# Optimization experiments

Hardware: AMD Instinct MI355X
Metric: run time of the kernel (lower is better)

## Reference

```python
import jax, jax.numpy as jnp
import numpy as np

SOS_TOKEN_ID = 1
SUMMARY_LEN = 16  # decoder produces SUMMARY_LEN - 1 steps


def setup_inputs() -> dict:
    key = jax.random.key(0)
    ks = jax.random.split(key, 10)
    B, L, D, Vc, Vs = 256, 200, 512, 50000, 20000
    s = 0.05  # keep activations in a sane range for tanh/softmax
    return {
        "method_code": jax.random.randint(ks[0], (B, L), 0, Vc),
        "code_emb_table": jax.random.normal(ks[1], (Vc, D), jnp.float32) * s,
        "summary_emb_table": jax.random.normal(ks[2], (Vs, D), jnp.float32) * s,
        "w_ih": jax.random.normal(ks[3], (4 * D, D), jnp.float32) * s,
        "w_hh": jax.random.normal(ks[4], (4 * D, D), jnp.float32) * s,
        "b_ih": jnp.zeros((4 * D,), jnp.float32),
        "b_hh": jnp.zeros((4 * D,), jnp.float32),
        "t_w": jax.random.normal(ks[5], (D, D), jnp.float32) * s,
        "t_b": jnp.zeros((D,), jnp.float32),
        "h_w": jax.random.normal(ks[6], (D, D), jnp.float32) * s,
        "h_b": jnp.zeros((D,), jnp.float32),
        "p_w": jax.random.normal(ks[7], (Vs, D), jnp.float32) * s,
        "p_b": jnp.zeros((Vs,), jnp.float32),
    }


def reference(method_code, code_emb_table, summary_emb_table,
              w_ih, w_hh, b_ih, b_hh, t_w, t_b, h_w, h_b, p_w, p_b):
    B = method_code.shape[0]
    D = code_emb_table.shape[1]
    code_emb = code_emb_table[method_code]  # [B, L, D]

    def step(carry, _):
        h, c, prev_tok = carry
        x = summary_emb_table[prev_tok]                       # [B, D]
        # torch LSTMCell: gates ordered i, f, g, o
        gates = x @ w_ih.T + b_ih + h @ w_hh.T + b_hh          # [B, 4D]
        i_g, f_g, g_g, o_g = jnp.split(gates, 4, axis=-1)
        c_new = jax.nn.sigmoid(f_g) * c + jax.nn.sigmoid(i_g) * jnp.tanh(g_g)
        h_new = jax.nn.sigmoid(o_g) * jnp.tanh(c_new)
        # dot-product attention over code embeddings
        attn = jax.nn.softmax(jnp.einsum('bd,bld->bl', h_new, code_emb), axis=-1)
        t = jnp.einsum('bl,bld->bd', attn, code_emb)           # [B, D]
        pre = t @ t_w.T + t_b + h_new @ h_w.T + h_b            # [B, D]
        logits = jnp.tanh(pre) @ p_w.T + p_b                   # [B, V]
        next_tok = jnp.argmax(logits, axis=-1)                 # greedy feedback
        return (h_new, c_new, next_tok), logits

    h0 = jnp.zeros((B, D), code_emb.dtype)
    c0 = jnp.zeros((B, D), code_emb.dtype)
    prev0 = jnp.full((B,), SOS_TOKEN_ID, dtype=method_code.dtype)
    _, logits_seq = jax.lax.scan(step, (h0, c0, prev0), None, length=SUMMARY_LEN - 1)
    return jnp.transpose(logits_seq, (1, 0, 2))  # [B, summary_len-1, V]
```

## Files before the change

### kernel.cpp

```cpp
#include <hip/hip_runtime.h>
#include <math.h>

#define BB 256
#define LL 200
#define DD 512
#define VS 20000
#define VS_PAD 20224
#define STEPS 15

typedef __attribute__((ext_vector_type(8))) short bf16x8;
typedef __attribute__((ext_vector_type(4))) float f32x4;

__device__ __forceinline__ unsigned int mono_key(float f) {
    unsigned int u = __float_as_uint(f);
    return (u & 0x80000000u) ? ~u : (u | 0x80000000u);
}

__device__ __forceinline__ unsigned short f2bf_rn(float x) {
    unsigned int u = __float_as_uint(x);
    unsigned int r = (u + 0x7FFFu + ((u >> 16) & 1u)) >> 16;
    return (unsigned short)r;
}
__device__ __forceinline__ float bf2f(unsigned short b) {
    return __uint_as_float((unsigned int)b << 16);
}

__device__ __forceinline__ void split_store8(float4 v0, float4 v1,
    unsigned short* __restrict__ hi, unsigned short* __restrict__ lo)
{
    ushort4 h0, h1, l0, l1;
    h0.x = f2bf_rn(v0.x); l0.x = f2bf_rn(v0.x - bf2f(h0.x));
    h0.y = f2bf_rn(v0.y); l0.y = f2bf_rn(v0.y - bf2f(h0.y));
    h0.z = f2bf_rn(v0.z); l0.z = f2bf_rn(v0.z - bf2f(h0.z));
    h0.w = f2bf_rn(v0.w); l0.w = f2bf_rn(v0.w - bf2f(h0.w));
    h1.x = f2bf_rn(v1.x); l1.x = f2bf_rn(v1.x - bf2f(h1.x));
    h1.y = f2bf_rn(v1.y); l1.y = f2bf_rn(v1.y - bf2f(h1.y));
    h1.z = f2bf_rn(v1.z); l1.z = f2bf_rn(v1.z - bf2f(h1.z));
    h1.w = f2bf_rn(v1.w); l1.w = f2bf_rn(v1.w - bf2f(h1.w));
    *(ushort4*)hi = h0; *(ushort4*)(hi + 4) = h1;
    *(ushort4*)lo = l0; *(ushort4*)(lo + 4) = l1;
}

__device__ __forceinline__ void split_frag(float4 v0, float4 v1, bf16x8& hi, bf16x8& lo)
{
    float vv[8] = {v0.x, v0.y, v0.z, v0.w, v1.x, v1.y, v1.z, v1.w};
    #pragma unroll
    for (int j = 0; j < 8; j++) {
        unsigned short hb = f2bf_rn(vv[j]);
        hi[j] = (short)hb;
        lo[j] = (short)f2bf_rn(vv[j] - bf2f(hb));
    }
}

__global__ __launch_bounds__(256) void init_keys_kernel(unsigned long long* keys) {
    keys[threadIdx.x] = (unsigned long long)(unsigned int)(~1u);
}


__global__ __launch_bounds__(256) void split_pw_kernel(
    const float* __restrict__ p_w, unsigned short* __restrict__ p_hi,
    unsigned short* __restrict__ p_lo)
{
    size_t q = (size_t)blockIdx.x * 256 + threadIdx.x;
    int P   = (int)(q >> 10);
    int rem = (int)(q & 1023);
    int c   = rem >> 6;
    int l   = rem & 63;
    int row = P * 16 + (l & 15);
    int ks  = c * 32 + (l >> 4) * 8;
    float4 v0 = {0.f, 0.f, 0.f, 0.f}, v1 = {0.f, 0.f, 0.f, 0.f};
    if (row < VS) {
        const float* src = p_w + (size_t)row * DD + ks;
        v0 = *(const float4*)src;
        v1 = *(const float4*)(src + 4);
    }
    split_store8(v0, v1, p_hi + q * 8, p_lo + q * 8);
}

template <int PERM>
__global__ __launch_bounds__(256) void split_wcat_kernel(
    const float* __restrict__ s0, const float* __restrict__ s1,
    unsigned short* __restrict__ wh, unsigned short* __restrict__ wl)
{
    size_t q = (size_t)blockIdx.x * 256 + threadIdx.x;
    int P   = (int)(q >> 11);
    int rem = (int)(q & 2047);
    int c   = rem >> 6;
    int l   = rem & 63;
    int row;
    if (PERM) row = (P & 3) * 512 + (P >> 2) * 16 + (l & 15);
    else      row = P * 16 + (l & 15);
    int k   = c * 32 + (l >> 4) * 8;
    const float* src = (k < 512) ? (s0 + (size_t)row * DD + k)
                                 : (s1 + (size_t)row * DD + (k - 512));
    float4 v0 = *(const float4*)src;
    float4 v1 = *(const float4*)(src + 4);
    split_store8(v0, v1, wh + q * 8, wl + q * 8);
}

__global__ __launch_bounds__(256) void gates_lstm_kernel(
    const float* __restrict__ sum_emb, const unsigned long long* __restrict__ keys,
    const unsigned short* __restrict__ hin_hi, const unsigned short* __restrict__ hin_lo,
    const unsigned short* __restrict__ w1h, const unsigned short* __restrict__ w1l,
    const float* __restrict__ bi, const float* __restrict__ bh,
    float* __restrict__ c, float* __restrict__ h,
    unsigned short* __restrict__ hout_hi, unsigned short* __restrict__ hout_lo)
{
    const int tid  = threadIdx.x;
    const int lane = tid & 63;
    const int wav  = tid >> 6;
    const int col = lane & 15;
    const int kg  = lane >> 4;
    const int m0  = (blockIdx.y * 4 + wav) * 16;
    const int nt  = blockIdx.x;

    unsigned int tok = ~(unsigned int)(keys[m0 + col] & 0xFFFFFFFFull);

    const size_t ahoff = (size_t)(m0 >> 4) * 8192 + (size_t)lane * 8;
    const size_t boff  = (size_t)(nt * 4) * 16384 + (size_t)lane * 8;

    f32x4 acc[4];
    #pragma unroll
    for (int g = 0; g < 4; g++) acc[g] = (f32x4){0.f, 0.f, 0.f, 0.f};

    bf16x8 fa_h[2], fa_l[2], fb_h[2][4], fb_l[2][4];

#define GL_LOAD(C, BUF)                                                            \
    {                                                                              \
        if ((C) < 16) {                                                            \
            const float* s_ = sum_emb + (size_t)tok * DD + (C) * 32 + kg * 8;      \
            float4 v0 = *(const float4*)s_;                                        \
            float4 v1 = *(const float4*)(s_ + 4);                                  \
            split_frag(v0, v1, fa_h[BUF], fa_l[BUF]);                              \
        } else {                                                                   \
            fa_h[BUF] = *(const bf16x8*)(hin_hi + ahoff + ((C) - 16) * 512);       \
            fa_l[BUF] = *(const bf16x8*)(hin_lo + ahoff + ((C) - 16) * 512);       \
        }                                                                          \
        _Pragma("unroll")                                                          \
        for (int g = 0; g < 4; g++) {                                              \
            fb_h[BUF][g] = *(const bf16x8*)(w1h + boff + (size_t)g * 16384 + (C) * 512); \
            fb_l[BUF][g] = *(const bf16x8*)(w1l + boff + (size_t)g * 16384 + (C) * 512); \
        }                                                                          \
    }

    GL_LOAD(0, 0);
    #pragma unroll
    for (int cc = 0; cc < 32; cc++) {
        const int cur = cc & 1, nxt = cur ^ 1;
        if (cc < 31) GL_LOAD(cc + 1, nxt);
        #pragma unroll
        for (int g = 0; g < 4; g++) {
            acc[g] = __builtin_amdgcn_mfma_f32_16x16x32_bf16(fa_h[cur], fb_h[cur][g], acc[g], 0, 0, 0);
            acc[g] = __builtin_amdgcn_mfma_f32_16x16x32_bf16(fa_h[cur], fb_l[cur][g], acc[g], 0, 0, 0);
            acc[g] = __builtin_amdgcn_mfma_f32_16x16x32_bf16(fa_l[cur], fb_h[cur][g], acc[g], 0, 0, 0);
        }
    }
#undef GL_LOAD

    const int feat = nt * 16 + col;
    float bias[4];
    #pragma unroll
    for (int g = 0; g < 4; g++)
        bias[g] = bi[g * 512 + feat] + bh[g * 512 + feat];

    #pragma unroll
    for (int r = 0; r < 4; r++) {
        const int b = m0 + kg * 4 + r;
        float vi = acc[0][r] + bias[0];
        float vf = acc[1][r] + bias[1];
        float vg = acc[2][r] + bias[2];
        float vo = acc[3][r] + bias[3];
        double ig = 1.0 / (1.0 + exp(-(double)vi));
        double fg = 1.0 / (1.0 + exp(-(double)vf));
        double gv = tanh((double)vg);
        double og = 1.0 / (1.0 + exp(-(double)vo));
        size_t cidx = (size_t)b * DD + feat;
        double cn = fg * (double)c[cidx] + ig * gv;
        double hn = og * tanh(cn);
        c[cidx] = (float)cn;
        float hf = (float)hn;
        h[cidx] = hf;
        size_t hidx = (size_t)(b >> 4) * 8192 + (size_t)(feat >> 5) * 512
                    + (size_t)(((feat >> 3) & 3) * 16 + (b & 15)) * 8 + (feat & 7);
        unsigned short hb2 = f2bf_rn(hf);
        hout_hi[hidx] = hb2;
        hout_lo[hidx] = f2bf_rn(hf - bf2f(hb2));
    }
}

__global__ __launch_bounds__(256) void pre_kernel(
    const unsigned short* __restrict__ t_hi, const unsigned short* __restrict__ t_lo,
    const unsigned short* __restrict__ h_hi, const unsigned short* __restrict__ h_lo,
    const unsigned short* __restrict__ w2h, const unsigned short* __restrict__ w2l,
    const float* __restrict__ tb, const float* __restrict__ hbv,
    unsigned short* __restrict__ o_hi, unsigned short* __restrict__ o_lo)
{
    const int tid  = threadIdx.x;
    const int lane = tid & 63;
    const int wav  = tid >> 6;
    const int col  = lane & 15;
    const int kg   = lane >> 4;
    const int m0   = blockIdx.y * 16;
    const int n0   = blockIdx.x * 32;

    const unsigned short* ah = (wav < 2) ? t_hi : h_hi;
    const unsigned short* al = (wav < 2) ? t_lo : h_lo;
    const size_t aoff = (size_t)(m0 >> 4) * 8192 + (size_t)lane * 8
                      + (size_t)((wav & 1) * 8) * 512;
    const size_t boff = (size_t)(n0 >> 4) * 16384 + (size_t)lane * 8
                      + (size_t)(wav * 8) * 512;

    f32x4 acc[2];
    acc[0] = (f32x4){0.f, 0.f, 0.f, 0.f};
    acc[1] = (f32x4){0.f, 0.f, 0.f, 0.f};

    bf16x8 fa_h[2], fa_l[2], fb_h[2][2], fb_l[2][2];
    fa_h[0] = *(const bf16x8*)(ah + aoff);
    fa_l[0] = *(const bf16x8*)(al + aoff);
    #pragma unroll
    for (int g = 0; g < 2; g++) {
        fb_h[0][g] = *(const bf16x8*)(w2h + boff + (size_t)g * 16384);
        fb_l[0][g] = *(const bf16x8*)(w2l + boff + (size_t)g * 16384);
    }
    #pragma unroll
    for (int cc = 0; cc < 8; cc++) {
        const int cur = cc & 1, nxt = cur ^ 1;
        if (cc < 7) {
            const int off = (cc + 1) * 512;
            fa_h[nxt] = *(const bf16x8*)(ah + aoff + off);
            fa_l[nxt] = *(const bf16x8*)(al + aoff + off);
            #pragma unroll
            for (int g = 0; g < 2; g++) {
                fb_h[nxt][g] = *(const bf16x8*)(w2h + boff + (size_t)g * 16384 + off);
                fb_l[nxt][g] = *(const bf16x8*)(w2l + boff + (size_t)g * 16384 + off);
            }
        }
        #pragma unroll
        for (int g = 0; g < 2; g++) {
            acc[g] = __builtin_amdgcn_mfma_f32_16x16x32_bf16(fa_h[cur], fb_h[cur][g], acc[g], 0, 0, 0);
            acc[g] = __builtin_amdgcn_mfma_f32_16x16x32_bf16(fa_h[cur], fb_l[cur][g], acc[g], 0, 0, 0);
            acc[g] = __builtin_amdgcn_mfma_f32_16x16x32_bf16(fa_l[cur], fb_h[cur][g], acc[g], 0, 0, 0);
        }
    }

    __shared__ float psum[4][16][32];
    #pragma unroll
    for (int g = 0; g < 2; g++)
        #pragma unroll
        for (int r = 0; r < 4; r++)
            psum[wav][kg * 4 + r][g * 16 + col] = acc[g][r];
    __syncthreads();

    #pragma unroll
    for (int e = 0; e < 2; e++) {
        const int idx  = tid * 2 + e;
        const int row  = idx >> 5, coln = idx & 31;
        const int b    = m0 + row;
        const int n    = n0 + coln;
        float accs = (psum[0][row][coln] + psum[1][row][coln])
                   + (psum[2][row][coln] + psum[3][row][coln]);
        float val = accs + (tb[n] + hbv[n]);
        float v2 = (float)tanh((double)val);
        int P = b >> 4, colb = b & 15;
        int cc2 = n >> 5, kgg = (n >> 3) & 3, jj = n & 7;
        size_t oidx = (size_t)P * 8192 + (size_t)cc2 * 512
                    + (size_t)(kgg * 16 + colb) * 8 + jj;
        unsigned short hb = f2bf_rn(v2);
        o_hi[oidx] = hb;
        o_lo[oidx] = f2bf_rn(v2 - bf2f(hb));
    }
}

template <int NCH, int EPI, int WPB>
__global__ __launch_bounds__(64 * WPB, 3) void mfma_gemm(
    const unsigned short* __restrict__ a0h, const unsigned short* __restrict__ a0l,
    const unsigned short* __restrict__ a1h, const unsigned short* __restrict__ a1l,
    const unsigned short* __restrict__ bmh, const unsigned short* __restrict__ bml,
    const float* __restrict__ bias0, const float* __restrict__ bias1,
    float* __restrict__ outp,
    unsigned short* __restrict__ o_hi, unsigned short* __restrict__ o_lo,
    unsigned long long* __restrict__ keys, int s)
{
    const int tid  = threadIdx.x;
    const int lane = tid & 63;
    const int wav  = tid >> 6;
    const int col = lane & 15;
    const int kg  = lane >> 4;
    const int m0 = (blockIdx.y * WPB + wav) * 32;
    const int n0 = blockIdx.x * 64;

    const size_t aoff = (size_t)(m0 >> 4) * 8192 + (size_t)lane * 8;
    const size_t boff = (size_t)(n0 >> 4) * (NCH * 512) + (size_t)lane * 8;

    f32x4 acc[2][4];
    #pragma unroll
    for (int f = 0; f < 2; f++)
        #pragma unroll
        for (int g = 0; g < 4; g++)
            acc[f][g] = (f32x4){0.f, 0.f, 0.f, 0.f};

    bf16x8 fah[2][2], fal[2][2], fbh[2][4], fbl[2][4];

#define LOAD_CHUNK(C, BUF)                                                         \
    {                                                                              \
        const unsigned short* ah_ = ((NCH == 16) || ((C) < 16)) ? a0h : a1h;       \
        const unsigned short* al_ = ((NCH == 16) || ((C) < 16)) ? a0l : a1l;       \
        const int cc_ = (C) & 15;                                                  \
        _Pragma("unroll")                                                          \
        for (int f = 0; f < 2; f++) {                                              \
            fah[BUF][f] = *(const bf16x8*)(ah_ + aoff + (size_t)f * 8192 + cc_ * 512); \
            fal[BUF][f] = *(const bf16x8*)(al_ + aoff + (size_t)f * 8192 + cc_ * 512); \
        }                                                                          \
        _Pragma("unroll")                                                          \
        for (int g = 0; g < 4; g++) {                                              \
            fbh[BUF][g] = *(const bf16x8*)(bmh + boff + (size_t)g * (NCH * 512) + (C) * 512); \
            fbl[BUF][g] = *(const bf16x8*)(bml + boff + (size_t)g * (NCH * 512) + (C) * 512); \
        }                                                                          \
    }

    LOAD_CHUNK(0, 0);
    #pragma unroll
    for (int c = 0; c < NCH; c++) {
        const int cur = c & 1, nxt = cur ^ 1;
        if (c < NCH - 1) LOAD_CHUNK(c + 1, nxt);
        #pragma unroll
        for (int f = 0; f < 2; f++)
            #pragma unroll
            for (int g = 0; g < 4; g++) {
                acc[f][g] = __builtin_amdgcn_mfma_f32_16x16x32_bf16(fah[cur][f], fbh[cur][g], acc[f][g], 0, 0, 0);
                acc[f][g] = __builtin_amdgcn_mfma_f32_16x16x32_bf16(fah[cur][f], fbl[cur][g], acc[f][g], 0, 0, 0);
                acc[f][g] = __builtin_amdgcn_mfma_f32_16x16x32_bf16(fal[cur][f], fbh[cur][g], acc[f][g], 0, 0, 0);
            }
    }
#undef LOAD_CHUNK

    float bias[4];
    #pragma unroll
    for (int g = 0; g < 4; g++) {
        int v = n0 + g * 16 + col;
        bias[g] = (v < VS) ? bias0[v] : 0.f;
    }

    #pragma unroll
    for (int f = 0; f < 2; f++) {
        #pragma unroll
        for (int r = 0; r < 4; r++) {
            const int b = m0 + f * 16 + kg * 4 + r;
            float* orow = outp + ((size_t)b * STEPS + s) * VS;
            unsigned long long kmax = 0ull;
            #pragma unroll
            for (int g = 0; g < 4; g++) {
                int v = n0 + g * 16 + col;
                float val = acc[f][g][r] + bias[g];
                if (v < VS) {
                    orow[v] = val;
                    unsigned long long key =
                        ((unsigned long long)mono_key(val) << 32) |
                        (unsigned long long)(unsigned int)(~v);
                    if (key > kmax) kmax = key;
                }
            }
            #pragma unroll
            for (int mk = 1; mk < 16; mk <<= 1) {
                unsigned long long o = __shfl_xor(kmax, mk, 64);
                if (o > kmax) kmax = o;
            }
            if (col == 0) {
                if (kmax > *(volatile unsigned long long*)&keys[b])
                    atomicMax(&keys[b], kmax);
            }
        }
    }
}

__global__ __launch_bounds__(512) void attn_kernel(
    const int* __restrict__ method_code, const float* __restrict__ code_emb,
    const float* __restrict__ h, unsigned short* __restrict__ t_hi,
    unsigned short* __restrict__ t_lo, unsigned long long* __restrict__ keys)
{
    const int b = blockIdx.x;
    const int tid = threadIdx.x;
    const int lane = tid & 63, wave = tid >> 6;

    __shared__ float sc[LL];
    __shared__ int   rows[LL];
    __shared__ float fred[256];
    __shared__ double dred[256];
    __shared__ float ts[DD];
    __shared__ float part[8][DD];

    if (tid < LL) rows[tid] = method_code[b * LL + tid];
    if (tid == 0) keys[b] = 0ull;
    const float* hb = h + (size_t)b * DD;
    float4 h0 = *(const float4*)(hb + lane * 8);
    float4 h1 = *(const float4*)(hb + lane * 8 + 4);
    __syncthreads();

    for (int l = wave; l < LL; l += 8) {
        const float* e = code_emb + (size_t)rows[l] * DD + lane * 8;
        float4 e0 = *(const float4*)e;
        float4 e1 = *(const float4*)(e + 4);
        float p = h0.x * e0.x + h0.y * e0.y + h0.z * e0.z + h0.w * e0.w
                + h1.x * e1.x + h1.y * e1.y + h1.z * e1.z + h1.w * e1.w;
        #pragma unroll
        for (int m = 1; m < 64; m <<= 1) p += __shfl_xor(p, m, 64);
        if (lane == 0) sc[l] = p;
    }
    __syncthreads();

    if (tid < 256) fred[tid] = (tid < LL) ? sc[tid] : -INFINITY;
    __syncthreads();
    for (int s2 = 128; s2 > 0; s2 >>= 1) {
        if (tid < s2) fred[tid] = fmaxf(fred[tid], fred[tid + s2]);
        __syncthreads();
    }
    float smax = fred[0];
    __syncthreads();
    double w = (tid < LL) ? exp((double)sc[tid] - (double)smax) : 0.0;
    if (tid < 256) dred[tid] = w;
    __syncthreads();
    for (int s2 = 128; s2 > 0; s2 >>= 1) {
        if (tid < s2) dred[tid] += dred[tid + s2];
        __syncthreads();
    }
    double ssum = dred[0];
    __syncthreads();
    if (tid < LL) sc[tid] = (float)(w / ssum);
    __syncthreads();

    float pa[8] = {0.f, 0.f, 0.f, 0.f, 0.f, 0.f, 0.f, 0.f};
    for (int l = wave; l < LL; l += 8) {
        float wl = sc[l];
        const float* e = code_emb + (size_t)rows[l] * DD + lane * 8;
        float4 e0 = *(const float4*)e;
        float4 e1 = *(const float4*)(e + 4);
        pa[0] = fmaf(wl, e0.x, pa[0]); pa[1] = fmaf(wl, e0.y, pa[1]);
        pa[2] = fmaf(wl, e0.z, pa[2]); pa[3] = fmaf(wl, e0.w, pa[3]);
        pa[4] = fmaf(wl, e1.x, pa[4]); pa[5] = fmaf(wl, e1.y, pa[5]);
        pa[6] = fmaf(wl, e1.z, pa[6]); pa[7] = fmaf(wl, e1.w, pa[7]);
    }
    #pragma unroll
    for (int j = 0; j < 8; j++) part[wave][lane * 8 + j] = pa[j];
    __syncthreads();

    {
        const int d = tid;
        float v01 = part[0][d] + part[1][d];
        float v23 = part[2][d] + part[3][d];
        float v45 = part[4][d] + part[5][d];
        float v67 = part[6][d] + part[7][d];
        ts[d] = (v01 + v23) + (v45 + v67);
    }
    __syncthreads();

    if (tid < 64) {
        const int cc = tid >> 2, kgg = tid & 3;
        const float* src = ts + cc * 32 + kgg * 8;
        float4 v0 = *(const float4*)src;
        float4 v1 = *(const float4*)(src + 4);
        size_t base = (size_t)(b >> 4) * 8192 + (size_t)cc * 512
                    + (size_t)(kgg * 16 + (b & 15)) * 8;
        split_store8(v0, v1, t_hi + base, t_lo + base);
    }
}

extern "C" void kernel_launch(void* const* d_in, const int* in_sizes, int n_in,
                              void* d_out, int out_size, void* d_ws, size_t ws_size,
                              hipStream_t stream)
{
    const int*   method_code = (const int*)d_in[0];
    const float* code_emb    = (const float*)d_in[1];
    const float* sum_emb     = (const float*)d_in[2];
    const float* w_ih        = (const float*)d_in[3];
    const float* w_hh        = (const float*)d_in[4];
    const float* b_ih        = (const float*)d_in[5];
    const float* b_hh        = (const float*)d_in[6];
    const float* t_w         = (const float*)d_in[7];
    const float* t_b         = (const float*)d_in[8];
    const float* h_w         = (const float*)d_in[9];
    const float* h_b         = (const float*)d_in[10];
    const float* p_w         = (const float*)d_in[11];
    const float* p_b         = (const float*)d_in[12];
    float* out = (float*)d_out;

    float* h     = (float*)d_ws;
    float* c     = h + BB * DD;
    unsigned long long* keys = (unsigned long long*)(c + BB * DD);
    unsigned short* a_hi   = (unsigned short*)(keys + BB);
    unsigned short* a_lo   = a_hi   + BB * DD;
    unsigned short* t_hi   = a_lo   + BB * DD;
    unsigned short* t_lo   = t_hi   + BB * DD;
    unsigned short* hp0_hi = t_lo   + BB * DD;
    unsigned short* hp0_lo = hp0_hi + BB * DD;
    unsigned short* hp1_hi = hp0_lo + BB * DD;
    unsigned short* hp1_lo = hp1_hi + BB * DD;
    unsigned short* w1_hi  = hp1_lo + BB * DD;
    unsigned short* w1_lo  = w1_hi  + (size_t)2048 * 1024;
    unsigned short* w2_hi  = w1_lo  + (size_t)2048 * 1024;
    unsigned short* w2_lo  = w2_hi  + (size_t)512 * 1024;
    unsigned short* p_hi   = w2_lo  + (size_t)512 * 1024;
    unsigned short* p_lo   = p_hi   + (size_t)VS_PAD * DD;

    hipMemsetAsync(h, 0, (size_t)2 * BB * DD * sizeof(float), stream);
    hipMemsetAsync(hp0_hi, 0, (size_t)2 * BB * DD * sizeof(unsigned short), stream);
    init_keys_kernel<<<1, 256, 0, stream>>>(keys);
    split_pw_kernel<<<(VS_PAD * 64) / 256, 256, 0, stream>>>(p_w, p_hi, p_lo);
    split_wcat_kernel<1><<<1024, 256, 0, stream>>>(w_ih, w_hh, w1_hi, w1_lo);
    split_wcat_kernel<0><<<256, 256, 0, stream>>>(t_w, h_w, w2_hi, w2_lo);

    for (int s = 0; s < STEPS; s++) {
        const unsigned short* hin_hi  = (s & 1) ? hp1_hi : hp0_hi;
        const unsigned short* hin_lo  = (s & 1) ? hp1_lo : hp0_lo;
        unsigned short*       hout_hi = (s & 1) ? hp0_hi : hp1_hi;
        unsigned short*       hout_lo = (s & 1) ? hp0_lo : hp1_lo;

        gates_lstm_kernel<<<dim3(32, 4), 256, 0, stream>>>(
            sum_emb, keys, hin_hi, hin_lo, w1_hi, w1_lo, b_ih, b_hh,
            c, h, hout_hi, hout_lo);
        attn_kernel<<<256, 512, 0, stream>>>(method_code, code_emb, h, t_hi, t_lo, keys);
        pre_kernel<<<dim3(16, 16), 256, 0, stream>>>(
            t_hi, t_lo, hout_hi, hout_lo, w2_hi, w2_lo, t_b, h_b, a_hi, a_lo);
        mfma_gemm<16, 2, 4><<<dim3(316, 2), 256, 0, stream>>>(
            a_hi, a_lo, nullptr, nullptr, p_hi, p_lo, p_b, nullptr,
            out, nullptr, nullptr, keys, s);
    }
}
```

Measured before the change: 2.068 ms.

## Fuse attention score and weighted-sum passes with online softmax

Replaces the two-pass attention (scores, block softmax reductions, then a second gather of code embeddings) with a single pass that keeps a running max and sum per wave and rescales the partial weighted sums. Per-wave partials are merged once at the end with exp rescaling. This removes the second read of 200 gathered embedding rows and the many barrier-heavy tree reductions. In exchange it adds per-iteration double-precision exp and conditional rescaling, and the float rounding order changes slightly.

```diff
diff --git a/kernel.cpp b/kernel.cpp
--- a/kernel.cpp
+++ b/kernel.cpp
@@ -382,12 +382,11 @@
     const int tid = threadIdx.x;
     const int lane = tid & 63, wave = tid >> 6;
 
-    __shared__ float sc[LL];
-    __shared__ int   rows[LL];
-    __shared__ float fred[256];
-    __shared__ double dred[256];
-    __shared__ float ts[DD];
-    __shared__ float part[8][DD];
+    __shared__ int    rows[LL];
+    __shared__ float  ts[DD];
+    __shared__ float  part[8][DD];
+    __shared__ float  wmax[8];
+    __shared__ double wsum[8];
 
     if (tid < LL) rows[tid] = method_code[b * LL + tid];
     if (tid == 0) keys[b] = 0ull;
@@ -396,6 +395,9 @@
     float4 h1 = *(const float4*)(hb + lane * 8 + 4);
     __syncthreads();
 
+    float  m = -INFINITY;
+    double s = 0.0;
+    float pa[8] = {0.f, 0.f, 0.f, 0.f, 0.f, 0.f, 0.f, 0.f};
     for (int l = wave; l < LL; l += 8) {
         const float* e = code_emb + (size_t)rows[l] * DD + lane * 8;
         float4 e0 = *(const float4*)e;
@@ -403,53 +405,44 @@
         float p = h0.x * e0.x + h0.y * e0.y + h0.z * e0.z + h0.w * e0.w
                 + h1.x * e1.x + h1.y * e1.y + h1.z * e1.z + h1.w * e1.w;
         #pragma unroll
-        for (int m = 1; m < 64; m <<= 1) p += __shfl_xor(p, m, 64);
-        if (lane == 0) sc[l] = p;
-    }
+        for (int mk = 1; mk < 64; mk <<= 1) p += __shfl_xor(p, mk, 64);
+        if (p > m) {
+            float scale = (m == -INFINITY) ? 0.f : (float)exp((double)m - (double)p);
+            s *= (double)scale;
+            #pragma unroll
+            for (int j = 0; j < 8; j++) pa[j] *= scale;
+            m = p;
+        }
+        double wd = exp((double)p - (double)m);
+        s += wd;
+        float wf = (float)wd;
+        pa[0] = fmaf(wf, e0.x, pa[0]); pa[1] = fmaf(wf, e0.y, pa[1]);
+        pa[2] = fmaf(wf, e0.z, pa[2]); pa[3] = fmaf(wf, e0.w, pa[3]);
+        pa[4] = fmaf(wf, e1.x, pa[4]); pa[5] = fmaf(wf, e1.y, pa[5]);
+        pa[6] = fmaf(wf, e1.z, pa[6]); pa[7] = fmaf(wf, e1.w, pa[7]);
+    }
+    #pragma unroll
+    for (int j = 0; j < 8; j++) part[wave][lane * 8 + j] = pa[j];
+    if (lane == 0) { wmax[wave] = m; wsum[wave] = s; }
     __syncthreads();
 
-    if (tid < 256) fred[tid] = (tid < LL) ? sc[tid] : -INFINITY;
-    __syncthreads();
-    for (int s2 = 128; s2 > 0; s2 >>= 1) {
-        if (tid < s2) fred[tid] = fmaxf(fred[tid], fred[tid + s2]);
-        __syncthreads();
-    }
-    float smax = fred[0];
-    __syncthreads();
-    double w = (tid < LL) ? exp((double)sc[tid] - (double)smax) : 0.0;
-    if (tid < 256) dred[tid] = w;
-    __syncthreads();
-    for (int s2 = 128; s2 > 0; s2 >>= 1) {
-        if (tid < s2) dred[tid] += dred[tid + s2];
-        __syncthreads();
-    }
-    double ssum = dred[0];
-    __syncthreads();
-    if (tid < LL) sc[tid] = (float)(w / ssum);
-    __syncthreads();
-
-    float pa[8] = {0.f, 0.f, 0.f, 0.f, 0.f, 0.f, 0.f, 0.f};
-    for (int l = wave; l < LL; l += 8) {
-        float wl = sc[l];
-        const float* e = code_emb + (size_t)rows[l] * DD + lane * 8;
-        float4 e0 = *(const float4*)e;
-        float4 e1 = *(const float4*)(e + 4);
-        pa[0] = fmaf(wl, e0.x, pa[0]); pa[1] = fmaf(wl, e0.y, pa[1]);
-        pa[2] = fmaf(wl, e0.z, pa[2]); pa[3] = fmaf(wl, e0.w, pa[3]);
-        pa[4] = fmaf(wl, e1.x, pa[4]); pa[5] = fmaf(wl, e1.y, pa[5]);
-        pa[6] = fmaf(wl, e1.z, pa[6]); pa[7] = fmaf(wl, e1.w, pa[7]);
-    }
-    #pragma unroll
-    for (int j = 0; j < 8; j++) part[wave][lane * 8 + j] = pa[j];
-    __syncthreads();
-
     {
+        float M = wmax[0];
+        #pragma unroll
+        for (int w2 = 1; w2 < 8; w2++) M = fmaxf(M, wmax[w2]);
+        float sc8[8];
+        double S = 0.0;
+        #pragma unroll
+        for (int w2 = 0; w2 < 8; w2++) {
+            sc8[w2] = (float)exp((double)wmax[w2] - (double)M);
+            S += wsum[w2] * (double)sc8[w2];
+        }
         const int d = tid;
-        float v01 = part[0][d] + part[1][d];
-        float v23 = part[2][d] + part[3][d];
-        float v45 = part[4][d] + part[5][d];
-        float v67 = part[6][d] + part[7][d];
-        ts[d] = (v01 + v23) + (v45 + v67);
+        float v01 = part[0][d] * sc8[0] + part[1][d] * sc8[1];
+        float v23 = part[2][d] * sc8[2] + part[3][d] * sc8[3];
+        float v45 = part[4][d] * sc8[4] + part[5][d] * sc8[5];
+        float v67 = part[6][d] * sc8[6] + part[7][d] * sc8[7];
+        ts[d] = (float)((double)((v01 + v23) + (v45 + v67)) / S);
     }
     __syncthreads();
 
```

Result: faster. 1.949 ms (-5.8%).
